# Performance work log

Hardware: AMD Instinct MI355X
Metric: run time of the kernel (lower is better)

## Reference

```python
import jax, jax.numpy as jnp
import numpy as np

N = 100_000          # nodes
E = 800_000          # edges
IN_DIM = 128
OUT_DIM = 128
H = 8                # heads
DK = OUT_DIM // H    # 16
T = 3                # node types
R = 8                # edge relation types
LN_EPS = 1e-5


def setup_inputs():
    key = jax.random.key(0)
    k = jax.random.split(key, 16)
    node_inp = jax.random.normal(k[0], (N, IN_DIM), dtype=jnp.float32)
    node_type = jax.random.randint(k[1], (N,), 0, T)
    edge_index = jax.random.randint(k[2], (2, E), 0, N)
    edge_type = jax.random.randint(k[3], (E,), 0, R)
    edge_sign = jax.random.randint(k[4], (E,), 0, 3) - 1      # values in {-1,0,1}
    edge_distance = jax.random.uniform(k[5], (E,), dtype=jnp.float32) * 2e5
    sc = 1.0 / np.sqrt(IN_DIM)
    Wq = jax.random.normal(k[6], (T, IN_DIM, OUT_DIM), dtype=jnp.float32) * sc
    Wk = jax.random.normal(k[7], (T, IN_DIM, OUT_DIM), dtype=jnp.float32) * sc
    Wv = jax.random.normal(k[8], (T, IN_DIM, OUT_DIM), dtype=jnp.float32) * sc
    bq = jnp.zeros((T, OUT_DIM), jnp.float32)
    bk = jnp.zeros((T, OUT_DIM), jnp.float32)
    bv = jnp.zeros((T, OUT_DIM), jnp.float32)
    rel_q = jax.random.normal(k[9], (R, H, DK), dtype=jnp.float32) * 0.2
    rel_k = jax.random.normal(k[10], (R, H, DK), dtype=jnp.float32) * 0.2
    rel_v = jax.random.normal(k[11], (R, H, DK), dtype=jnp.float32) * 0.2
    rel_bias = jnp.zeros((R, H), jnp.float32)
    ones = jnp.ones((H, DK), dtype=jnp.float32)
    sign_k_fixed = jnp.stack([-ones, ones], axis=0)   # [2,H,DK] buffers (neg,pos)
    sign_v_fixed = jnp.stack([-ones, ones], axis=0)
    sign_k_neutral = jnp.ones((H, DK), jnp.float32)
    sign_v_neutral = jnp.ones((H, DK), jnp.float32)
    dist_alpha = jnp.float32(0.1)
    dist_tau = jnp.float32(1e5)
    skip = jnp.ones((T,), jnp.float32)
    ln_gamma = jnp.ones((T, OUT_DIM), jnp.float32)
    ln_beta = jnp.zeros((T, OUT_DIM), jnp.float32)
    return dict(node_inp=node_inp, node_type=node_type, edge_index=edge_index,
                edge_type=edge_type, edge_sign=edge_sign, edge_distance=edge_distance,
                Wq=Wq, bq=bq, Wk=Wk, bk=bk, Wv=Wv, bv=bv,
                rel_q=rel_q, rel_k=rel_k, rel_v=rel_v, rel_bias=rel_bias,
                sign_k_fixed=sign_k_fixed, sign_v_fixed=sign_v_fixed,
                sign_k_neutral=sign_k_neutral, sign_v_neutral=sign_v_neutral,
                dist_alpha=dist_alpha, dist_tau=dist_tau, skip=skip,
                ln_gamma=ln_gamma, ln_beta=ln_beta)


def reference(node_inp, node_type, edge_index, edge_type, edge_sign, edge_distance,
              Wq, bq, Wk, bk, Wv, bv, rel_q, rel_k, rel_v, rel_bias,
              sign_k_fixed, sign_v_fixed, sign_k_neutral, sign_v_neutral,
              dist_alpha, dist_tau, skip, ln_gamma, ln_beta):
    src, dst = edge_index[0], edge_index[1]
    n = node_inp.shape[0]
    e = src.shape[0]
    # Per-node-type Q/K/V: compute projections for all types [N,T,O], select by type
    # (equivalent to the masked per-type Linear dispatch in the torch code).
    ar = jnp.arange(n)
    Q = (jnp.einsum('nd,tdo->nto', node_inp, Wq) + bq)[ar, node_type].reshape(n, H, DK)
    K = (jnp.einsum('nd,tdo->nto', node_inp, Wk) + bk)[ar, node_type].reshape(n, H, DK)
    V = (jnp.einsum('nd,tdo->nto', node_inp, Wv) + bv)[ar, node_type].reshape(n, H, DK)
    # sign dispatch: -1 -> 0 (neg), +1 -> 1 (pos), anything else -> 2 (neutral)
    sign_idx = jnp.where(edge_sign == -1, 0, jnp.where(edge_sign == 1, 1, 2))
    sign_k_all = jnp.concatenate([sign_k_fixed, sign_k_neutral[None]], axis=0)  # [3,H,DK]
    sign_v_all = jnp.concatenate([sign_v_fixed, sign_v_neutral[None]], axis=0)
    # edge-wise gather + relational modulation
    q_eff = Q[dst] * rel_q[edge_type]                               # [E,H,DK]
    k_eff = K[src] * rel_k[edge_type] * sign_k_all[sign_idx]
    v_eff = V[src] * rel_v[edge_type] * sign_v_all[sign_idx]
    scores = jnp.sum(q_eff * k_eff, axis=-1) / np.sqrt(DK)          # [E,H]
    scores = scores + rel_bias[edge_type]
    phi = dist_alpha * jnp.exp(-edge_distance / (dist_tau + 1e-9))
    scores = scores + phi[:, None]
    # segment softmax over destination nodes
    m = jax.ops.segment_max(scores, dst, num_segments=n)            # [N,H]
    m = jax.lax.stop_gradient(jnp.where(jnp.isfinite(m), m, 0.0))
    es = jnp.exp(scores - m[dst])
    Z = jax.ops.segment_sum(es, dst, num_segments=n)
    attn = es / (Z[dst] + 1e-9)
    # message scatter-aggregate
    msg = (v_eff * attn[:, :, None]).reshape(e, OUT_DIM)
    out = jax.ops.segment_sum(msg, dst, num_segments=n)             # [N,OUT_DIM]
    # per-type gated residual + per-type LayerNorm
    alpha = jax.nn.sigmoid(skip)[node_type][:, None]
    x = alpha * out + (1.0 - alpha) * node_inp
    mu = jnp.mean(x, axis=-1, keepdims=True)
    var = jnp.mean((x - mu) ** 2, axis=-1, keepdims=True)
    xn = (x - mu) * jax.lax.rsqrt(var + LN_EPS)
    return xn * ln_gamma[node_type] + ln_beta[node_type]
```

## Files before the change

kernel.cpp:

```cpp
#include <hip/hip_runtime.h>
#include <hip/hip_bf16.h>

typedef unsigned int uint;
typedef unsigned short ushort;
typedef unsigned long long ull;
typedef __attribute__((ext_vector_type(8))) short short8;
typedef __attribute__((ext_vector_type(4))) float f32x4;

#define WP_ELEMS 147456

__device__ __forceinline__ float bf2f(ushort u) { return __uint_as_float(((uint)u) << 16); }
__device__ __forceinline__ ushort f2bf(float f) {
  uint x = __float_as_uint(f);
  return (ushort)((x + 0x7fffu + ((x >> 16) & 1u)) >> 16);
}
__device__ __forceinline__ uint packbf(float a, float b) {
  return ((uint)f2bf(b) << 16) | (uint)f2bf(a);
}

__global__ __launch_bounds__(256) void cvt_kernel(
    const float* __restrict__ wq, const float* __restrict__ wk, const float* __restrict__ wv,
    const float* __restrict__ rq, const float* __restrict__ rk, const float* __restrict__ rv,
    const float* __restrict__ skf, const float* __restrict__ svf,
    const float* __restrict__ skn, const float* __restrict__ svn,
    ushort* __restrict__ Wp, float* __restrict__ rkv) {
  int i = blockIdx.x * 256 + threadIdx.x;
  if (i < WP_ELEMS) {
    int j    = i & 7;
    int lane = (i >> 3) & 63;
    int ot   = (i >> 9) & 7;
    int ks   = (i >> 12) & 3;
    int mt   = i >> 14;
    int mat  = mt / 3;
    int t    = mt - mat * 3;
    int o = ot * 16 + (lane & 15);
    int d = ks * 32 + (lane >> 4) * 8 + j;
    const float* src = (mat == 0) ? wq : (mat == 1) ? wk : wv;
    Wp[i] = f2bf(src[t * 16384 + d * 128 + o]);
  }
  if (i < 3072) {
    int comb = i >> 7, c = i & 127;
    int et = comb / 3, sidx = comb - et * 3;
    float skv = (sidx < 2) ? skf[sidx * 128 + c] : skn[c];
    float svv = (sidx < 2) ? svf[sidx * 128 + c] : svn[c];
    float kkv = 0.25f * rq[et * 128 + c] * rk[et * 128 + c] * skv;
    float vvv = rv[et * 128 + c] * svv;
    int base = comb * 256 + (c >> 1) * 4 + (c & 1);
    rkv[base] = kkv;
    rkv[base + 2] = vvv;
  }
}

__global__ __launch_bounds__(256) void count_kernel(const int* __restrict__ ntype,
                                                    int* __restrict__ cnt, int N) {
  int i = blockIdx.x * 256 + threadIdx.x;
  int lane = threadIdx.x & 63;
  int t = (i < N) ? ntype[i] : -1;
#pragma unroll
  for (int tt = 0; tt < 3; ++tt) {
    ull mask = __ballot(t == tt);
    if (mask) {
      int leader = __ffsll((long long)mask) - 1;
      if (lane == leader) atomicAdd(&cnt[tt], __popcll(mask));
    }
  }
}

__global__ void offs_kernel(const int* __restrict__ cnt, int* __restrict__ off) {
  int o = 0;
  off[0] = 0;
  for (int t = 0; t < 3; ++t) {
    o += ((cnt[t] + 63) >> 6) << 6;
    off[t + 1] = o;
  }
}

__global__ __launch_bounds__(256) void fill_kernel(const int* __restrict__ ntype,
                                                   const int* __restrict__ off,
                                                   int* __restrict__ pos,
                                                   int* __restrict__ perm,
                                                   int* __restrict__ pinv, int N) {
  int i = blockIdx.x * 256 + threadIdx.x;
  int lane = threadIdx.x & 63;
  int t = (i < N) ? ntype[i] : -1;
#pragma unroll
  for (int tt = 0; tt < 3; ++tt) {
    ull mask = __ballot(t == tt);
    if (mask) {
      int leader = __ffsll((long long)mask) - 1;
      int base = 0;
      if (lane == leader) base = atomicAdd(&pos[tt], __popcll(mask));
      base = __shfl(base, leader);
      if (t == tt) {
        int rank = __popcll(mask & ((lane == 63) ? 0x7fffffffffffffffull
                                                 : ((1ull << lane) - 1ull)));
        int p = off[tt] + base + rank;
        perm[p] = i;
        pinv[i] = p;
      }
    }
  }
}

__global__ __launch_bounds__(256) void gemm_kernel(
    const float* __restrict__ X, const int* __restrict__ perm,
    const int* __restrict__ off, const ushort* __restrict__ Wp,
    const float* __restrict__ bq, const float* __restrict__ bk, const float* __restrict__ bv,
    float* __restrict__ Qp, uint* __restrict__ KVp) {
  __shared__ __align__(16) char smem[33792];
  __shared__ int prow[64];
  ushort* As = (ushort*)smem;
  float* tbuf = (float*)smem;
  const int tid = threadIdx.x;
  const int base = blockIdx.x * 64;
  const int off1 = off[1], off2 = off[2], off3 = off[3];
  if (base >= off3) return;
  const int t = (base >= off1) + (base >= off2);

  if (tid < 64) prow[tid] = perm[base + tid];
  __syncthreads();
#pragma unroll
  for (int pass = 0; pass < 8; ++pass) {
    int row = pass * 8 + (tid >> 5);
    int dw = tid & 31;
    int p = prow[row];
    uint ux = 0u, uy = 0u;
    if (p >= 0) {
      float4 xv = *(const float4*)(X + (size_t)p * 128 + dw * 4);
      ux = packbf(xv.x, xv.y);
      uy = packbf(xv.z, xv.w);
    }
    uint* s = (uint*)smem + row * 68 + dw * 2;
    s[0] = ux; s[1] = uy;
  }
  __syncthreads();

  const int lane = tid & 63;
  const int w = tid >> 6;
  const int m0 = w * 16;
  const int r = lane & 15;
  const int q = lane >> 4;

  short8 afrag[4];
#pragma unroll
  for (int ks = 0; ks < 4; ++ks)
    afrag[ks] = *(const short8*)(As + (m0 + r) * 136 + ks * 32 + q * 8);
  __syncthreads();

  float* tw = tbuf + w * 2112;
  uint4 ksave[4];
#pragma unroll
  for (int mat = 0; mat < 3; ++mat) {
    f32x4 acc[8];
#pragma unroll
    for (int ot = 0; ot < 8; ++ot) acc[ot] = (f32x4){0.f, 0.f, 0.f, 0.f};

    const ushort* wb = Wp + (size_t)(mat * 3 + t) * 16384 + lane * 8;
#pragma unroll
    for (int ks = 0; ks < 4; ++ks) {
      const ushort* wk_ = wb + ks * 4096;
#pragma unroll
      for (int ot = 0; ot < 8; ++ot) {
        short8 b = *(const short8*)(wk_ + ot * 512);
        acc[ot] = __builtin_amdgcn_mfma_f32_16x16x32_bf16(afrag[ks], b, acc[ot], 0, 0, 0);
      }
    }

    const float* bias = (mat == 0) ? bq : (mat == 1) ? bk : bv;
#pragma unroll
    for (int ot = 0; ot < 8; ++ot) {
      float bi = bias[t * 128 + ot * 16 + r];
#pragma unroll
      for (int reg = 0; reg < 4; ++reg)
        tw[(q * 4 + reg) * 132 + ot * 16 + r] = acc[ot][reg] + bi;
    }
    if (mat == 0) {
#pragma unroll
      for (int p = 0; p < 8; ++p) {
        int f = (p * 64 + lane) * 4;
        int row = f >> 7, col = f & 127;
        float4 val = *(const float4*)(tw + row * 132 + col);
        *(float4*)(Qp + (size_t)(base + m0 + row) * 128 + col) = val;
      }
    } else if (mat == 1) {
#pragma unroll
      for (int p = 0; p < 4; ++p) {
        int g = p * 64 + lane;
        int f = g * 8;
        int row = f >> 7, col = f & 127;
        const float* src = tw + row * 132 + col;
        float4 a4 = *(const float4*)(src);
        float4 b4 = *(const float4*)(src + 4);
        uint4 u;
        u.x = packbf(a4.x, a4.y);
        u.y = packbf(a4.z, a4.w);
        u.z = packbf(b4.x, b4.y);
        u.w = packbf(b4.z, b4.w);
        ksave[p] = u;
      }
    } else {
#pragma unroll
      for (int p = 0; p < 4; ++p) {
        int g = p * 64 + lane;
        int f = g * 8;
        int row = f >> 7, col = f & 127;
        const float* src = tw + row * 132 + col;
        float4 a4 = *(const float4*)(src);
        float4 b4 = *(const float4*)(src + 4);
        uint4 v4;
        v4.x = packbf(a4.x, a4.y);
        v4.y = packbf(a4.z, a4.w);
        v4.z = packbf(b4.x, b4.y);
        v4.w = packbf(b4.z, b4.w);
        uint4 w0, w1;
        w0.x = ksave[p].x; w0.y = v4.x; w0.z = ksave[p].y; w0.w = v4.y;
        w1.x = ksave[p].z; w1.y = v4.z; w1.z = ksave[p].w; w1.w = v4.w;
        uint* dstp = KVp + (size_t)(base + m0 + row) * 128 + col;
        *(uint4*)(dstp) = w0;
        *(uint4*)(dstp + 4) = w1;
      }
    }
  }
}

__global__ __launch_bounds__(256) void ecount_kernel(const int* __restrict__ edst,
                                                     int* __restrict__ ecnt, int E) {
  int e = blockIdx.x * 256 + threadIdx.x;
  if (e < E) atomicAdd(&ecnt[edst[e]], 1);
}

__global__ __launch_bounds__(256) void csum_kernel(const int* __restrict__ ecnt,
                                                   int* __restrict__ csum, int N) {
  __shared__ int s[4];
  int basei = blockIdx.x * 1024;
  int tid = threadIdx.x;
  int v = 0;
#pragma unroll
  for (int k = 0; k < 4; ++k) {
    int i = basei + k * 256 + tid;
    if (i < N) v += ecnt[i];
  }
#pragma unroll
  for (int m = 1; m < 64; m <<= 1) v += __shfl_xor(v, m);
  if ((tid & 63) == 0) s[tid >> 6] = v;
  __syncthreads();
  if (tid == 0) csum[blockIdx.x] = s[0] + s[1] + s[2] + s[3];
}

__global__ __launch_bounds__(1024) void cscan_kernel(const int* __restrict__ csum,
                                                     int* __restrict__ coff,
                                                     int* __restrict__ rowptrN,
                                                     int NC, int E) {
  __shared__ int sd[32];
  int tid = threadIdx.x, lane = tid & 63, w = tid >> 6;
  int v = (tid < NC) ? csum[tid] : 0;
  int x = v;
#pragma unroll
  for (int d = 1; d < 64; d <<= 1) {
    int t = __shfl_up(x, d);
    if (lane >= d) x += t;
  }
  if (lane == 63) sd[w] = x;
  __syncthreads();
  if (w == 0 && lane < 16) {
    int y = sd[lane];
#pragma unroll
    for (int d = 1; d < 16; d <<= 1) {
      int t = __shfl_up(y, d);
      if (lane >= d) y += t;
    }
    sd[16 + lane] = y;
  }
  __syncthreads();
  int excl = ((w > 0) ? sd[16 + w - 1] : 0) + (x - v);
  if (tid < NC) coff[tid] = excl;
  if (tid == 0) rowptrN[0] = E;
}

__global__ __launch_bounds__(1024) void rowptr_kernel(const int* __restrict__ ecnt,
                                                      const int* __restrict__ coff,
                                                      int* __restrict__ rowptr,
                                                      int* __restrict__ cursor, int N) {
  __shared__ int sd[32];
  int basei = blockIdx.x * 1024;
  int tid = threadIdx.x, lane = tid & 63, w = tid >> 6;
  int i = basei + tid;
  int v = (i < N) ? ecnt[i] : 0;
  int x = v;
#pragma unroll
  for (int d = 1; d < 64; d <<= 1) {
    int t = __shfl_up(x, d);
    if (lane >= d) x += t;
  }
  if (lane == 63) sd[w] = x;
  __syncthreads();
  if (w == 0 && lane < 16) {
    int y = sd[lane];
#pragma unroll
    for (int d = 1; d < 16; d <<= 1) {
      int t = __shfl_up(y, d);
      if (lane >= d) y += t;
    }
    sd[16 + lane] = y;
  }
  __syncthreads();
  int excl = coff[blockIdx.x] + ((w > 0) ? sd[16 + w - 1] : 0) + (x - v);
  if (i < N) { rowptr[i] = excl; cursor[i] = excl; }
}

__global__ __launch_bounds__(256) void scatter_kernel(
    const int* __restrict__ esrc, const int* __restrict__ edst,
    const int* __restrict__ etype, const int* __restrict__ esign,
    const float* __restrict__ edist,
    const float* __restrict__ p_alpha, const float* __restrict__ p_tau,
    const int* __restrict__ pinv, int* __restrict__ cursor,
    int* __restrict__ esrc_s, int* __restrict__ emeta_s, float* __restrict__ ephi_s, int E) {
  int e = blockIdx.x * 256 + threadIdx.x;
  if (e >= E) return;
  int dst = edst[e];
  int p = atomicAdd(&cursor[dst], 1);
  int et = etype[e], sg = esign[e];
  int sidx = (sg == -1) ? 0 : ((sg == 1) ? 1 : 2);
  float parg = fminf(fmaxf(-edist[e] / (p_tau[0] + 1e-9f), -80.f), 0.f);
  esrc_s[p] = pinv[esrc[e]];
  emeta_s[p] = (et << 8) | (et * 3 + sidx);
  ephi_s[p] = p_alpha[0] * __expf(parg);
}

__global__ __launch_bounds__(256) void agg_kernel(
    const float* __restrict__ Qp, const uint* __restrict__ KVp,
    const int* __restrict__ pinv, const int* __restrict__ rowptr,
    const int* __restrict__ esrc_s, const int* __restrict__ emeta_s,
    const float* __restrict__ ephi_s,
    const float* __restrict__ rb, const float* __restrict__ rkv,
    const float* __restrict__ X, const int* __restrict__ ntype,
    const float* __restrict__ skip, const float* __restrict__ gamma,
    const float* __restrict__ beta, float* __restrict__ y, int N) {
  int dst = blockIdx.x * 4 + (threadIdx.x >> 6);
  if (dst >= N) return;
  int lane = threadIdx.x & 63;
  int c = lane * 2;
  int h = lane >> 3;

  int pq = pinv[dst];
  float2 qv = *(const float2*)(Qp + (size_t)pq * 128 + c);
  float accx = 0.f, accy = 0.f;
  float z = 0.f;

  int row0 = rowptr[dst], row1 = rowptr[dst + 1];
  for (int bb = row0; bb < row1; bb += 64) {
    int n = min(64, row1 - bb);
    int srcv = 0, metav = 0;
    float phiv = 0.f;
    if (lane < n) {
      srcv = esrc_s[bb + lane];
      metav = emeta_s[bb + lane];
      phiv = ephi_s[bb + lane];
    }
    for (int it0 = 0; it0 < n; it0 += 8) {
      int m = min(8, n - it0);
      uint2 kv[8];
#pragma unroll
      for (int j = 0; j < 8; ++j) {
        if (j < m) {
          int pe = __shfl(srcv, it0 + j);
          kv[j] = *(const uint2*)(KVp + (size_t)pe * 128 + lane * 2);
        }
      }
#pragma unroll
      for (int j = 0; j < 8; ++j) {
        if (j < m) {
          int meta = __shfl(metav, it0 + j);
          float phi = __shfl(phiv, it0 + j);
          int comb = meta & 255;
          int et = meta >> 8;
          float4 tb = *(const float4*)(rkv + comb * 256 + lane * 4);
          float kx = __uint_as_float(kv[j].x << 16);
          float ky = __uint_as_float(kv[j].x & 0xffff0000u);
          float vx = __uint_as_float(kv[j].y << 16);
          float vy = __uint_as_float(kv[j].y & 0xffff0000u);
          float part = qv.x * kx * tb.x;
          part = fmaf(qv.y * ky, tb.y, part);
          part += __shfl_xor(part, 1);
          part += __shfl_xor(part, 2);
          part += __shfl_xor(part, 4);
          float score = fminf(part + rb[et * 8 + h] + phi, 80.f);
          float es = __expf(score);
          z += es;
          accx = fmaf(es, vx * tb.z, accx);
          accy = fmaf(es, vy * tb.w, accy);
        }
      }
    }
  }

  float inv = 1.0f / (z + 1e-9f);
  float o0 = accx * inv, o1 = accy * inv;

  int t = ntype[dst];
  float a = 1.0f / (1.0f + __expf(-skip[t]));
  float2 xv = *(const float2*)(X + (size_t)dst * 128 + c);
  float v0 = a * o0 + (1.0f - a) * xv.x;
  float v1 = a * o1 + (1.0f - a) * xv.y;

  float sum = v0 + v1, sq = v0 * v0 + v1 * v1;
#pragma unroll
  for (int m = 1; m < 64; m <<= 1) {
    sum += __shfl_xor(sum, m);
    sq  += __shfl_xor(sq, m);
  }
  float mean = sum * (1.0f / 128.0f);
  float var = fmaxf(sq * (1.0f / 128.0f) - mean * mean, 0.0f);
  float rstd = rsqrtf(var + 1e-5f);

  float g0 = gamma[t * 128 + c], g1 = gamma[t * 128 + c + 1];
  float b0 = beta[t * 128 + c],  b1 = beta[t * 128 + c + 1];
  float2 o;
  o.x = (v0 - mean) * rstd * g0 + b0;
  o.y = (v1 - mean) * rstd * g1 + b1;
  *(float2*)(y + (size_t)dst * 128 + c) = o;
}

extern "C" void kernel_launch(void* const* d_in, const int* in_sizes, int n_in,
                              void* d_out, int out_size, void* d_ws, size_t ws_size,
                              hipStream_t stream) {
  const float* X     = (const float*)d_in[0];
  const int*   ntype = (const int*)d_in[1];
  const int*   eidx  = (const int*)d_in[2];
  const int*   etype = (const int*)d_in[3];
  const int*   esign = (const int*)d_in[4];
  const float* edist = (const float*)d_in[5];
  const float* wq = (const float*)d_in[6];
  const float* bq = (const float*)d_in[7];
  const float* wk = (const float*)d_in[8];
  const float* bk = (const float*)d_in[9];
  const float* wv = (const float*)d_in[10];
  const float* bv = (const float*)d_in[11];
  const float* rq = (const float*)d_in[12];
  const float* rk = (const float*)d_in[13];
  const float* rv = (const float*)d_in[14];
  const float* rb = (const float*)d_in[15];

  const int N = in_sizes[1];
  const int E = in_sizes[3];
  const int NP = N + 192;
  const int NC = (N + 1023) / 1024;

  float* ws = (float*)d_ws;
  float* Qp   = ws;
  uint*  KVp  = (uint*)(Qp + (size_t)NP * 128);
  float* rkv  = (float*)(KVp + (size_t)NP * 128);
  ushort* Wp  = (ushort*)(rkv + 6144);
  int* cnt    = (int*)(Wp + WP_ELEMS);
  int* pos    = cnt + 4;
  int* ecnt   = pos + 4;
  int* perm   = ecnt + N;
  int* pinv   = perm + NP;
  int* off    = pinv + N;
  int* rowptr = off + 4;
  int* cursor = rowptr + N + 1;
  int* csum   = cursor + N;
  int* coff   = csum + 1024;
  int* esrc_s = coff + 1024;
  int* emeta_s = esrc_s + E;
  float* ephi_s = (float*)(emeta_s + E);

  hipMemsetAsync(cnt, 0, (size_t)(8 + N) * sizeof(int), stream);
  hipMemsetAsync(perm, 0xFF, (size_t)NP * sizeof(int), stream);

  cvt_kernel<<<(WP_ELEMS + 255) / 256, 256, 0, stream>>>(
      wq, wk, wv, rq, rk, rv, (const float*)d_in[16], (const float*)d_in[17],
      (const float*)d_in[18], (const float*)d_in[19], Wp, rkv);
  count_kernel<<<(N + 255) / 256, 256, 0, stream>>>(ntype, cnt, N);
  offs_kernel<<<1, 1, 0, stream>>>(cnt, off);
  fill_kernel<<<(N + 255) / 256, 256, 0, stream>>>(ntype, off, pos, perm, pinv, N);

  ecount_kernel<<<(E + 255) / 256, 256, 0, stream>>>(eidx + E, ecnt, E);
  csum_kernel<<<NC, 256, 0, stream>>>(ecnt, csum, N);
  cscan_kernel<<<1, 1024, 0, stream>>>(csum, coff, rowptr + N, NC, E);
  rowptr_kernel<<<NC, 1024, 0, stream>>>(ecnt, coff, rowptr, cursor, N);
  scatter_kernel<<<(E + 255) / 256, 256, 0, stream>>>(
      eidx, eidx + E, etype, esign, edist, (const float*)d_in[20], (const float*)d_in[21],
      pinv, cursor, esrc_s, emeta_s, ephi_s, E);

  gemm_kernel<<<(N + 255) / 64, 256, 0, stream>>>(X, perm, off, Wp, bq, bk, bv, Qp, KVp);

  agg_kernel<<<(N + 3) / 4, 256, 0, stream>>>(Qp, KVp, pinv, rowptr, esrc_s, emeta_s,
                                              ephi_s, rb, rkv, X, ntype,
                                              (const float*)d_in[22], (const float*)d_in[23],
                                              (const float*)d_in[24], (float*)d_out, N);
}
```

Before: 588.0 us.

## Process four edges per wave concurrently with wide loads and software prefetch

The aggregation kernel now splits each 64-lane wave into four 16-lane groups, and each group handles a different edge. Each lane owns 8 channels, loaded with 16-byte vectors instead of 2-channel loads. A register double-buffered prefetch fetches the next edge's K/V and relation tables while the current edge is computed. Partial sums are then combined across the groups with shuffles, and only 16 lanes do the LayerNorm epilogue. This cuts the per-edge shuffle reductions and exposed gather latency, at the cost of more registers and idle lanes on low-degree nodes.

```diff
diff --git a/kernel.cpp b/kernel.cpp
--- a/kernel.cpp
+++ b/kernel.cpp
@@ -17,6 +17,8 @@
 __device__ __forceinline__ uint packbf(float a, float b) {
   return ((uint)f2bf(b) << 16) | (uint)f2bf(a);
 }
+__device__ __forceinline__ float bflo(uint u) { return __uint_as_float(u << 16); }
+__device__ __forceinline__ float bfhi(uint u) { return __uint_as_float(u & 0xffff0000u); }
 
 __global__ __launch_bounds__(256) void cvt_kernel(
     const float* __restrict__ wq, const float* __restrict__ wk, const float* __restrict__ wv,
@@ -327,6 +329,73 @@
   ephi_s[p] = p_alpha[0] * __expf(parg);
 }
 
+struct Pass {
+  uint4 kv0, kv1;
+  float4 t0, t1, t2, t3;
+  float bias;
+  int valid;
+};
+
+__device__ __forceinline__ Pass prefetch_pass(
+    int idx, int n, int srcv, int metav, float phiv,
+    const uint* __restrict__ KVp, const float* __restrict__ rkv,
+    const float* __restrict__ rb, int cl) {
+  Pass P;
+  P.valid = (idx < n);
+  int pe = __shfl(srcv, idx);
+  int meta = __shfl(metav, idx);
+  float phi = __shfl(phiv, idx);
+  if (!P.valid) { pe = 0; meta = 0; phi = 0.f; }
+  int comb = meta & 255;
+  int et = meta >> 8;
+  const uint* kvb = KVp + (size_t)pe * 128 + cl * 8;
+  P.kv0 = *(const uint4*)(kvb);
+  P.kv1 = *(const uint4*)(kvb + 4);
+  const float* tb = rkv + comb * 256 + cl * 16;
+  P.t0 = *(const float4*)(tb);
+  P.t1 = *(const float4*)(tb + 4);
+  P.t2 = *(const float4*)(tb + 8);
+  P.t3 = *(const float4*)(tb + 12);
+  P.bias = rb[et * 8 + (cl >> 1)] + phi;
+  return P;
+}
+
+__device__ __forceinline__ void compute_pass(
+    const Pass& P, const float4& q0, const float4& q1, float& z,
+    float& a0, float& a1, float& a2, float& a3,
+    float& a4, float& a5, float& a6, float& a7) {
+  float k0 = bflo(P.kv0.x), k1 = bfhi(P.kv0.x);
+  float v0 = bflo(P.kv0.y), v1 = bfhi(P.kv0.y);
+  float k2 = bflo(P.kv0.z), k3 = bfhi(P.kv0.z);
+  float v2 = bflo(P.kv0.w), v3 = bfhi(P.kv0.w);
+  float k4 = bflo(P.kv1.x), k5 = bfhi(P.kv1.x);
+  float v4 = bflo(P.kv1.y), v5 = bfhi(P.kv1.y);
+  float k6 = bflo(P.kv1.z), k7 = bfhi(P.kv1.z);
+  float v6 = bflo(P.kv1.w), v7 = bfhi(P.kv1.w);
+
+  float part = q0.x * (k0 * P.t0.x);
+  part = fmaf(q0.y, k1 * P.t0.y, part);
+  part = fmaf(q0.z, k2 * P.t1.x, part);
+  part = fmaf(q0.w, k3 * P.t1.y, part);
+  part = fmaf(q1.x, k4 * P.t2.x, part);
+  part = fmaf(q1.y, k5 * P.t2.y, part);
+  part = fmaf(q1.z, k6 * P.t3.x, part);
+  part = fmaf(q1.w, k7 * P.t3.y, part);
+  part += __shfl_xor(part, 1);
+  float score = fminf(part + P.bias, 80.f);
+  float es = __expf(score);
+  es = P.valid ? es : 0.f;
+  z += es;
+  a0 = fmaf(es, v0 * P.t0.z, a0);
+  a1 = fmaf(es, v1 * P.t0.w, a1);
+  a2 = fmaf(es, v2 * P.t1.z, a2);
+  a3 = fmaf(es, v3 * P.t1.w, a3);
+  a4 = fmaf(es, v4 * P.t2.z, a4);
+  a5 = fmaf(es, v5 * P.t2.w, a5);
+  a6 = fmaf(es, v6 * P.t3.z, a6);
+  a7 = fmaf(es, v7 * P.t3.w, a7);
+}
+
 __global__ __launch_bounds__(256) void agg_kernel(
     const float* __restrict__ Qp, const uint* __restrict__ KVp,
     const int* __restrict__ pinv, const int* __restrict__ rowptr,
@@ -339,12 +408,17 @@
   int dst = blockIdx.x * 4 + (threadIdx.x >> 6);
   if (dst >= N) return;
   int lane = threadIdx.x & 63;
-  int c = lane * 2;
-  int h = lane >> 3;
+  int g = lane >> 4;
+  int cl = lane & 15;
+  int c0 = cl * 8;
 
   int pq = pinv[dst];
-  float2 qv = *(const float2*)(Qp + (size_t)pq * 128 + c);
-  float accx = 0.f, accy = 0.f;
+  const float* qb = Qp + (size_t)pq * 128 + c0;
+  float4 q0 = *(const float4*)(qb);
+  float4 q1 = *(const float4*)(qb + 4);
+
+  float a0 = 0.f, a1 = 0.f, a2 = 0.f, a3 = 0.f;
+  float a4 = 0.f, a5 = 0.f, a6 = 0.f, a7 = 0.f;
   float z = 0.f;
 
   int row0 = rowptr[dst], row1 = rowptr[dst + 1];
@@ -357,68 +431,78 @@
       metav = emeta_s[bb + lane];
       phiv = ephi_s[bb + lane];
     }
-    for (int it0 = 0; it0 < n; it0 += 8) {
-      int m = min(8, n - it0);
-      uint2 kv[8];
-#pragma unroll
-      for (int j = 0; j < 8; ++j) {
-        if (j < m) {
-          int pe = __shfl(srcv, it0 + j);
-          kv[j] = *(const uint2*)(KVp + (size_t)pe * 128 + lane * 2);
-        }
+    int np = (n + 3) >> 2;
+    Pass A = prefetch_pass(g, n, srcv, metav, phiv, KVp, rkv, rb, cl);
+    int p = 0;
+    while (true) {
+      if (p + 1 < np) {
+        Pass B = prefetch_pass((p + 1) * 4 + g, n, srcv, metav, phiv, KVp, rkv, rb, cl);
+        compute_pass(A, q0, q1, z, a0, a1, a2, a3, a4, a5, a6, a7);
+        A = B;
+        ++p;
+      } else {
+        compute_pass(A, q0, q1, z, a0, a1, a2, a3, a4, a5, a6, a7);
+        break;
       }
-#pragma unroll
-      for (int j = 0; j < 8; ++j) {
-        if (j < m) {
-          int meta = __shfl(metav, it0 + j);
-          float phi = __shfl(phiv, it0 + j);
-          int comb = meta & 255;
-          int et = meta >> 8;
-          float4 tb = *(const float4*)(rkv + comb * 256 + lane * 4);
-          float kx = __uint_as_float(kv[j].x << 16);
-          float ky = __uint_as_float(kv[j].x & 0xffff0000u);
-          float vx = __uint_as_float(kv[j].y << 16);
-          float vy = __uint_as_float(kv[j].y & 0xffff0000u);
-          float part = qv.x * kx * tb.x;
-          part = fmaf(qv.y * ky, tb.y, part);
-          part += __shfl_xor(part, 1);
-          part += __shfl_xor(part, 2);
-          part += __shfl_xor(part, 4);
-          float score = fminf(part + rb[et * 8 + h] + phi, 80.f);
-          float es = __expf(score);
-          z += es;
-          accx = fmaf(es, vx * tb.z, accx);
-          accy = fmaf(es, vy * tb.w, accy);
-        }
-      }
-    }
-  }
-
-  float inv = 1.0f / (z + 1e-9f);
-  float o0 = accx * inv, o1 = accy * inv;
-
-  int t = ntype[dst];
-  float a = 1.0f / (1.0f + __expf(-skip[t]));
-  float2 xv = *(const float2*)(X + (size_t)dst * 128 + c);
-  float v0 = a * o0 + (1.0f - a) * xv.x;
-  float v1 = a * o1 + (1.0f - a) * xv.y;
-
-  float sum = v0 + v1, sq = v0 * v0 + v1 * v1;
-#pragma unroll
-  for (int m = 1; m < 64; m <<= 1) {
-    sum += __shfl_xor(sum, m);
-    sq  += __shfl_xor(sq, m);
-  }
-  float mean = sum * (1.0f / 128.0f);
-  float var = fmaxf(sq * (1.0f / 128.0f) - mean * mean, 0.0f);
-  float rstd = rsqrtf(var + 1e-5f);
-
-  float g0 = gamma[t * 128 + c], g1 = gamma[t * 128 + c + 1];
-  float b0 = beta[t * 128 + c],  b1 = beta[t * 128 + c + 1];
-  float2 o;
-  o.x = (v0 - mean) * rstd * g0 + b0;
-  o.y = (v1 - mean) * rstd * g1 + b1;
-  *(float2*)(y + (size_t)dst * 128 + c) = o;
+    }
+  }
+
+#pragma unroll
+  for (int m = 16; m < 64; m <<= 1) {
+    a0 += __shfl_xor(a0, m); a1 += __shfl_xor(a1, m);
+    a2 += __shfl_xor(a2, m); a3 += __shfl_xor(a3, m);
+    a4 += __shfl_xor(a4, m); a5 += __shfl_xor(a5, m);
+    a6 += __shfl_xor(a6, m); a7 += __shfl_xor(a7, m);
+    z  += __shfl_xor(z, m);
+  }
+
+  if (lane < 16) {
+    float inv = 1.0f / (z + 1e-9f);
+    float o0 = a0 * inv, o1 = a1 * inv, o2 = a2 * inv, o3 = a3 * inv;
+    float o4 = a4 * inv, o5 = a5 * inv, o6 = a6 * inv, o7 = a7 * inv;
+
+    int t = ntype[dst];
+    float a = 1.0f / (1.0f + __expf(-skip[t]));
+    float b = 1.0f - a;
+    const float* xb = X + (size_t)dst * 128 + c0;
+    float4 x0 = *(const float4*)(xb);
+    float4 x1 = *(const float4*)(xb + 4);
+    float w0 = a * o0 + b * x0.x, w1 = a * o1 + b * x0.y;
+    float w2 = a * o2 + b * x0.z, w3 = a * o3 + b * x0.w;
+    float w4 = a * o4 + b * x1.x, w5 = a * o5 + b * x1.y;
+    float w6 = a * o6 + b * x1.z, w7 = a * o7 + b * x1.w;
+
+    float sum = w0 + w1 + w2 + w3 + w4 + w5 + w6 + w7;
+    float sq = w0 * w0 + w1 * w1 + w2 * w2 + w3 * w3 +
+               w4 * w4 + w5 * w5 + w6 * w6 + w7 * w7;
+#pragma unroll
+    for (int m = 1; m < 16; m <<= 1) {
+      sum += __shfl_xor(sum, m);
+      sq  += __shfl_xor(sq, m);
+    }
+    float mean = sum * (1.0f / 128.0f);
+    float var = fmaxf(sq * (1.0f / 128.0f) - mean * mean, 0.0f);
+    float rstd = rsqrtf(var + 1e-5f);
+
+    const float* gb = gamma + t * 128 + c0;
+    const float* bb2 = beta + t * 128 + c0;
+    float4 g0 = *(const float4*)(gb);
+    float4 g1 = *(const float4*)(gb + 4);
+    float4 be0 = *(const float4*)(bb2);
+    float4 be1 = *(const float4*)(bb2 + 4);
+    float4 r0, r1;
+    r0.x = (w0 - mean) * rstd * g0.x + be0.x;
+    r0.y = (w1 - mean) * rstd * g0.y + be0.y;
+    r0.z = (w2 - mean) * rstd * g0.z + be0.z;
+    r0.w = (w3 - mean) * rstd * g0.w + be0.w;
+    r1.x = (w4 - mean) * rstd * g1.x + be1.x;
+    r1.y = (w5 - mean) * rstd * g1.y + be1.y;
+    r1.z = (w6 - mean) * rstd * g1.z + be1.z;
+    r1.w = (w7 - mean) * rstd * g1.w + be1.w;
+    float* yb = y + (size_t)dst * 128 + c0;
+    *(float4*)(yb) = r0;
+    *(float4*)(yb + 4) = r1;
+  }
 }
 
 extern "C" void kernel_launch(void* const* d_in, const int* in_sizes, int n_in,
```

Result: no change. 585.8 us (-0.4%).

## Process eight edges per wave with lanes owning full heads in aggregation

Applied to the files above, without the earlier changes.

The aggregation kernel is remapped so each group of eight lanes handles one edge and each lane owns a full 16-channel head. The per-head dot product is then computed in-lane, with no per-edge shuffle reduction, and K/V rows are read as wide 16-byte loads. Partial accumulators are combined across the eight edge groups once at the end. Edge source and metadata are packed into one int, which saves one gather stream, and the relation tables are split into separate K and V arrays. The costs are more registers per lane, a larger final cross-lane reduction, and a packed index that assumes node indices fit in 18 bits.

```diff
diff --git a/kernel.cpp b/kernel.cpp
--- a/kernel.cpp
+++ b/kernel.cpp
@@ -9,7 +9,6 @@
 
 #define WP_ELEMS 147456
 
-__device__ __forceinline__ float bf2f(ushort u) { return __uint_as_float(((uint)u) << 16); }
 __device__ __forceinline__ ushort f2bf(float f) {
   uint x = __float_as_uint(f);
   return (ushort)((x + 0x7fffu + ((x >> 16) & 1u)) >> 16);
@@ -17,13 +16,15 @@
 __device__ __forceinline__ uint packbf(float a, float b) {
   return ((uint)f2bf(b) << 16) | (uint)f2bf(a);
 }
+__device__ __forceinline__ float bflo(uint u) { return __uint_as_float(u << 16); }
+__device__ __forceinline__ float bfhi(uint u) { return __uint_as_float(u & 0xffff0000u); }
 
 __global__ __launch_bounds__(256) void cvt_kernel(
     const float* __restrict__ wq, const float* __restrict__ wk, const float* __restrict__ wv,
     const float* __restrict__ rq, const float* __restrict__ rk, const float* __restrict__ rv,
     const float* __restrict__ skf, const float* __restrict__ svf,
     const float* __restrict__ skn, const float* __restrict__ svn,
-    ushort* __restrict__ Wp, float* __restrict__ rkv) {
+    ushort* __restrict__ Wp, float* __restrict__ rkk, float* __restrict__ rvv) {
   int i = blockIdx.x * 256 + threadIdx.x;
   if (i < WP_ELEMS) {
     int j    = i & 7;
@@ -43,11 +44,8 @@
     int et = comb / 3, sidx = comb - et * 3;
     float skv = (sidx < 2) ? skf[sidx * 128 + c] : skn[c];
     float svv = (sidx < 2) ? svf[sidx * 128 + c] : svn[c];
-    float kkv = 0.25f * rq[et * 128 + c] * rk[et * 128 + c] * skv;
-    float vvv = rv[et * 128 + c] * svv;
-    int base = comb * 256 + (c >> 1) * 4 + (c & 1);
-    rkv[base] = kkv;
-    rkv[base + 2] = vvv;
+    rkk[i] = 0.25f * rq[et * 128 + c] * rk[et * 128 + c] * skv;
+    rvv[i] = rv[et * 128 + c] * svv;
   }
 }
 
@@ -314,7 +312,7 @@
     const float* __restrict__ edist,
     const float* __restrict__ p_alpha, const float* __restrict__ p_tau,
     const int* __restrict__ pinv, int* __restrict__ cursor,
-    int* __restrict__ esrc_s, int* __restrict__ emeta_s, float* __restrict__ ephi_s, int E) {
+    int* __restrict__ epk_s, float* __restrict__ ephi_s, int E) {
   int e = blockIdx.x * 256 + threadIdx.x;
   if (e >= E) return;
   int dst = edst[e];
@@ -322,90 +320,147 @@
   int et = etype[e], sg = esign[e];
   int sidx = (sg == -1) ? 0 : ((sg == 1) ? 1 : 2);
   float parg = fminf(fmaxf(-edist[e] / (p_tau[0] + 1e-9f), -80.f), 0.f);
-  esrc_s[p] = pinv[esrc[e]];
-  emeta_s[p] = (et << 8) | (et * 3 + sidx);
+  epk_s[p] = pinv[esrc[e]] | ((et * 3 + sidx) << 18) | (et << 23);
   ephi_s[p] = p_alpha[0] * __expf(parg);
 }
 
 __global__ __launch_bounds__(256) void agg_kernel(
     const float* __restrict__ Qp, const uint* __restrict__ KVp,
     const int* __restrict__ pinv, const int* __restrict__ rowptr,
-    const int* __restrict__ esrc_s, const int* __restrict__ emeta_s,
-    const float* __restrict__ ephi_s,
-    const float* __restrict__ rb, const float* __restrict__ rkv,
+    const int* __restrict__ epk_s, const float* __restrict__ ephi_s,
+    const float* __restrict__ rb, const float* __restrict__ rkk,
+    const float* __restrict__ rvv,
     const float* __restrict__ X, const int* __restrict__ ntype,
     const float* __restrict__ skip, const float* __restrict__ gamma,
     const float* __restrict__ beta, float* __restrict__ y, int N) {
   int dst = blockIdx.x * 4 + (threadIdx.x >> 6);
   if (dst >= N) return;
-  int lane = threadIdx.x & 63;
-  int c = lane * 2;
-  int h = lane >> 3;
+  const int lane = threadIdx.x & 63;
+  const int g = lane >> 3;
+  const int h = lane & 7;
+  const int cb = h * 16;
 
   int pq = pinv[dst];
-  float2 qv = *(const float2*)(Qp + (size_t)pq * 128 + c);
-  float accx = 0.f, accy = 0.f;
+  const float* qb = Qp + (size_t)pq * 128 + cb;
+  float4 q0 = *(const float4*)(qb);
+  float4 q1 = *(const float4*)(qb + 4);
+  float4 q2 = *(const float4*)(qb + 8);
+  float4 q3 = *(const float4*)(qb + 12);
+
+  float4 A0 = {0.f, 0.f, 0.f, 0.f}, A1 = A0, A2 = A0, A3 = A0;
   float z = 0.f;
 
   int row0 = rowptr[dst], row1 = rowptr[dst + 1];
   for (int bb = row0; bb < row1; bb += 64) {
     int n = min(64, row1 - bb);
-    int srcv = 0, metav = 0;
+    int pkv = 0;
     float phiv = 0.f;
     if (lane < n) {
-      srcv = esrc_s[bb + lane];
-      metav = emeta_s[bb + lane];
+      pkv = epk_s[bb + lane];
       phiv = ephi_s[bb + lane];
     }
-    for (int it0 = 0; it0 < n; it0 += 8) {
-      int m = min(8, n - it0);
-      uint2 kv[8];
-#pragma unroll
-      for (int j = 0; j < 8; ++j) {
-        if (j < m) {
-          int pe = __shfl(srcv, it0 + j);
-          kv[j] = *(const uint2*)(KVp + (size_t)pe * 128 + lane * 2);
-        }
-      }
-#pragma unroll
-      for (int j = 0; j < 8; ++j) {
-        if (j < m) {
-          int meta = __shfl(metav, it0 + j);
-          float phi = __shfl(phiv, it0 + j);
-          int comb = meta & 255;
-          int et = meta >> 8;
-          float4 tb = *(const float4*)(rkv + comb * 256 + lane * 4);
-          float kx = __uint_as_float(kv[j].x << 16);
-          float ky = __uint_as_float(kv[j].x & 0xffff0000u);
-          float vx = __uint_as_float(kv[j].y << 16);
-          float vy = __uint_as_float(kv[j].y & 0xffff0000u);
-          float part = qv.x * kx * tb.x;
-          part = fmaf(qv.y * ky, tb.y, part);
-          part += __shfl_xor(part, 1);
-          part += __shfl_xor(part, 2);
-          part += __shfl_xor(part, 4);
-          float score = fminf(part + rb[et * 8 + h] + phi, 80.f);
-          float es = __expf(score);
-          z += es;
-          accx = fmaf(es, vx * tb.z, accx);
-          accy = fmaf(es, vy * tb.w, accy);
-        }
-      }
-    }
+    int np = (n + 7) >> 3;
+    for (int p = 0; p < np; ++p) {
+      int idx = p * 8 + g;
+      int pk = __shfl(pkv, idx);
+      float phi = __shfl(phiv, idx);
+      int pe = pk & 0x3ffff;
+      int comb = (pk >> 18) & 31;
+      int et = (pk >> 23) & 7;
+      const uint* kvb = KVp + (size_t)pe * 128 + h * 16;
+      uint4 c0 = *(const uint4*)(kvb);
+      uint4 c1 = *(const uint4*)(kvb + 4);
+      uint4 c2 = *(const uint4*)(kvb + 8);
+      uint4 c3 = *(const uint4*)(kvb + 12);
+      const float* kkb = rkk + comb * 128 + cb;
+      float4 t0 = *(const float4*)(kkb);
+      float4 t1 = *(const float4*)(kkb + 4);
+      float4 t2 = *(const float4*)(kkb + 8);
+      float4 t3 = *(const float4*)(kkb + 12);
+      float sA = q0.x * t0.x * bflo(c0.x);
+      sA = fmaf(q0.y * t0.y, bfhi(c0.x), sA);
+      sA = fmaf(q0.z * t0.z, bflo(c0.z), sA);
+      sA = fmaf(q0.w * t0.w, bfhi(c0.z), sA);
+      float sB = q1.x * t1.x * bflo(c1.x);
+      sB = fmaf(q1.y * t1.y, bfhi(c1.x), sB);
+      sB = fmaf(q1.z * t1.z, bflo(c1.z), sB);
+      sB = fmaf(q1.w * t1.w, bfhi(c1.z), sB);
+      float sC = q2.x * t2.x * bflo(c2.x);
+      sC = fmaf(q2.y * t2.y, bfhi(c2.x), sC);
+      sC = fmaf(q2.z * t2.z, bflo(c2.z), sC);
+      sC = fmaf(q2.w * t2.w, bfhi(c2.z), sC);
+      float sD = q3.x * t3.x * bflo(c3.x);
+      sD = fmaf(q3.y * t3.y, bfhi(c3.x), sD);
+      sD = fmaf(q3.z * t3.z, bflo(c3.z), sD);
+      sD = fmaf(q3.w * t3.w, bfhi(c3.z), sD);
+      float score = (sA + sB) + (sC + sD) + rb[et * 8 + h] + phi;
+      score = fminf(score, 80.f);
+      float es = (idx < n) ? __expf(score) : 0.f;
+      z += es;
+      const float* vvb = rvv + comb * 128 + cb;
+      float4 v0 = *(const float4*)(vvb);
+      float4 v1 = *(const float4*)(vvb + 4);
+      float4 v2 = *(const float4*)(vvb + 8);
+      float4 v3 = *(const float4*)(vvb + 12);
+      A0.x = fmaf(es, bflo(c0.y) * v0.x, A0.x);
+      A0.y = fmaf(es, bfhi(c0.y) * v0.y, A0.y);
+      A0.z = fmaf(es, bflo(c0.w) * v0.z, A0.z);
+      A0.w = fmaf(es, bfhi(c0.w) * v0.w, A0.w);
+      A1.x = fmaf(es, bflo(c1.y) * v1.x, A1.x);
+      A1.y = fmaf(es, bfhi(c1.y) * v1.y, A1.y);
+      A1.z = fmaf(es, bflo(c1.w) * v1.z, A1.z);
+      A1.w = fmaf(es, bfhi(c1.w) * v1.w, A1.w);
+      A2.x = fmaf(es, bflo(c2.y) * v2.x, A2.x);
+      A2.y = fmaf(es, bfhi(c2.y) * v2.y, A2.y);
+      A2.z = fmaf(es, bflo(c2.w) * v2.z, A2.z);
+      A2.w = fmaf(es, bfhi(c2.w) * v2.w, A2.w);
+      A3.x = fmaf(es, bflo(c3.y) * v3.x, A3.x);
+      A3.y = fmaf(es, bfhi(c3.y) * v3.y, A3.y);
+      A3.z = fmaf(es, bflo(c3.w) * v3.z, A3.z);
+      A3.w = fmaf(es, bfhi(c3.w) * v3.w, A3.w);
+    }
+  }
+
+#pragma unroll
+  for (int m = 8; m < 64; m <<= 1) {
+    A0.x += __shfl_xor(A0.x, m); A0.y += __shfl_xor(A0.y, m);
+    A0.z += __shfl_xor(A0.z, m); A0.w += __shfl_xor(A0.w, m);
+    A1.x += __shfl_xor(A1.x, m); A1.y += __shfl_xor(A1.y, m);
+    A1.z += __shfl_xor(A1.z, m); A1.w += __shfl_xor(A1.w, m);
+    A2.x += __shfl_xor(A2.x, m); A2.y += __shfl_xor(A2.y, m);
+    A2.z += __shfl_xor(A2.z, m); A2.w += __shfl_xor(A2.w, m);
+    A3.x += __shfl_xor(A3.x, m); A3.y += __shfl_xor(A3.y, m);
+    A3.z += __shfl_xor(A3.z, m); A3.w += __shfl_xor(A3.w, m);
+    z += __shfl_xor(z, m);
   }
 
   float inv = 1.0f / (z + 1e-9f);
-  float o0 = accx * inv, o1 = accy * inv;
-
   int t = ntype[dst];
   float a = 1.0f / (1.0f + __expf(-skip[t]));
-  float2 xv = *(const float2*)(X + (size_t)dst * 128 + c);
-  float v0 = a * o0 + (1.0f - a) * xv.x;
-  float v1 = a * o1 + (1.0f - a) * xv.y;
-
-  float sum = v0 + v1, sq = v0 * v0 + v1 * v1;
-#pragma unroll
-  for (int m = 1; m < 64; m <<= 1) {
+  float b = 1.0f - a;
+  const float* xb = X + (size_t)dst * 128 + cb;
+  float4 x0 = *(const float4*)(xb);
+  float4 x1 = *(const float4*)(xb + 4);
+  float4 x2 = *(const float4*)(xb + 8);
+  float4 x3 = *(const float4*)(xb + 12);
+  float4 W0, W1, W2, W3;
+  W0.x = a * (A0.x * inv) + b * x0.x; W0.y = a * (A0.y * inv) + b * x0.y;
+  W0.z = a * (A0.z * inv) + b * x0.z; W0.w = a * (A0.w * inv) + b * x0.w;
+  W1.x = a * (A1.x * inv) + b * x1.x; W1.y = a * (A1.y * inv) + b * x1.y;
+  W1.z = a * (A1.z * inv) + b * x1.z; W1.w = a * (A1.w * inv) + b * x1.w;
+  W2.x = a * (A2.x * inv) + b * x2.x; W2.y = a * (A2.y * inv) + b * x2.y;
+  W2.z = a * (A2.z * inv) + b * x2.z; W2.w = a * (A2.w * inv) + b * x2.w;
+  W3.x = a * (A3.x * inv) + b * x3.x; W3.y = a * (A3.y * inv) + b * x3.y;
+  W3.z = a * (A3.z * inv) + b * x3.z; W3.w = a * (A3.w * inv) + b * x3.w;
+
+  float sum = (W0.x + W0.y + W0.z + W0.w) + (W1.x + W1.y + W1.z + W1.w) +
+              (W2.x + W2.y + W2.z + W2.w) + (W3.x + W3.y + W3.z + W3.w);
+  float sq = (W0.x * W0.x + W0.y * W0.y + W0.z * W0.z + W0.w * W0.w) +
+             (W1.x * W1.x + W1.y * W1.y + W1.z * W1.z + W1.w * W1.w) +
+             (W2.x * W2.x + W2.y * W2.y + W2.z * W2.z + W2.w * W2.w) +
+             (W3.x * W3.x + W3.y * W3.y + W3.z * W3.z + W3.w * W3.w);
+#pragma unroll
+  for (int m = 1; m < 8; m <<= 1) {
     sum += __shfl_xor(sum, m);
     sq  += __shfl_xor(sq, m);
   }
@@ -413,12 +468,18 @@
   float var = fmaxf(sq * (1.0f / 128.0f) - mean * mean, 0.0f);
   float rstd = rsqrtf(var + 1e-5f);
 
-  float g0 = gamma[t * 128 + c], g1 = gamma[t * 128 + c + 1];
-  float b0 = beta[t * 128 + c],  b1 = beta[t * 128 + c + 1];
-  float2 o;
-  o.x = (v0 - mean) * rstd * g0 + b0;
-  o.y = (v1 - mean) * rstd * g1 + b1;
-  *(float2*)(y + (size_t)dst * 128 + c) = o;
+  if (g < 4) {
+    int c4 = cb + g * 4;
+    float4 Wg = (g == 0) ? W0 : (g == 1) ? W1 : (g == 2) ? W2 : W3;
+    float4 gm = *(const float4*)(gamma + t * 128 + c4);
+    float4 bt = *(const float4*)(beta + t * 128 + c4);
+    float4 r;
+    r.x = (Wg.x - mean) * rstd * gm.x + bt.x;
+    r.y = (Wg.y - mean) * rstd * gm.y + bt.y;
+    r.z = (Wg.z - mean) * rstd * gm.z + bt.z;
+    r.w = (Wg.w - mean) * rstd * gm.w + bt.w;
+    *(float4*)(y + (size_t)dst * 128 + c4) = r;
+  }
 }
 
 extern "C" void kernel_launch(void* const* d_in, const int* in_sizes, int n_in,
@@ -449,8 +510,9 @@
   float* ws = (float*)d_ws;
   float* Qp   = ws;
   uint*  KVp  = (uint*)(Qp + (size_t)NP * 128);
-  float* rkv  = (float*)(KVp + (size_t)NP * 128);
-  ushort* Wp  = (ushort*)(rkv + 6144);
+  float* rkk  = (float*)(KVp + (size_t)NP * 128);
+  float* rvv  = rkk + 3072;
+  ushort* Wp  = (ushort*)(rvv + 3072);
   int* cnt    = (int*)(Wp + WP_ELEMS);
   int* pos    = cnt + 4;
   int* ecnt   = pos + 4;
@@ -461,16 +523,15 @@
   int* cursor = rowptr + N + 1;
   int* csum   = cursor + N;
   int* coff   = csum + 1024;
-  int* esrc_s = coff + 1024;
-  int* emeta_s = esrc_s + E;
-  float* ephi_s = (float*)(emeta_s + E);
+  int* epk_s  = coff + 1024;
+  float* ephi_s = (float*)(epk_s + E);
 
   hipMemsetAsync(cnt, 0, (size_t)(8 + N) * sizeof(int), stream);
   hipMemsetAsync(perm, 0xFF, (size_t)NP * sizeof(int), stream);
 
   cvt_kernel<<<(WP_ELEMS + 255) / 256, 256, 0, stream>>>(
       wq, wk, wv, rq, rk, rv, (const float*)d_in[16], (const float*)d_in[17],
-      (const float*)d_in[18], (const float*)d_in[19], Wp, rkv);
+      (const float*)d_in[18], (const float*)d_in[19], Wp, rkk, rvv);
   count_kernel<<<(N + 255) / 256, 256, 0, stream>>>(ntype, cnt, N);
   offs_kernel<<<1, 1, 0, stream>>>(cnt, off);
   fill_kernel<<<(N + 255) / 256, 256, 0, stream>>>(ntype, off, pos, perm, pinv, N);
@@ -481,12 +542,12 @@
   rowptr_kernel<<<NC, 1024, 0, stream>>>(ecnt, coff, rowptr, cursor, N);
   scatter_kernel<<<(E + 255) / 256, 256, 0, stream>>>(
       eidx, eidx + E, etype, esign, edist, (const float*)d_in[20], (const float*)d_in[21],
-      pinv, cursor, esrc_s, emeta_s, ephi_s, E);
+      pinv, cursor, epk_s, ephi_s, E);
 
   gemm_kernel<<<(N + 255) / 64, 256, 0, stream>>>(X, perm, off, Wp, bq, bk, bv, Qp, KVp);
 
-  agg_kernel<<<(N + 3) / 4, 256, 0, stream>>>(Qp, KVp, pinv, rowptr, esrc_s, emeta_s,
-                                              ephi_s, rb, rkv, X, ntype,
+  agg_kernel<<<(N + 3) / 4, 256, 0, stream>>>(Qp, KVp, pinv, rowptr, epk_s, ephi_s,
+                                              rb, rkk, rvv, X, ntype,
                                               (const float*)d_in[22], (const float*)d_in[23],
                                               (const float*)d_in[24], (float*)d_out, N);
 }
```

Result: slower. 604.1 us (+2.7%).
